# Kernel optimization log

Hardware: AMD Instinct MI355X
Metric: run time of the kernel (lower is better)

Reference implementation:

```python
import jax, jax.numpy as jnp
import numpy as np
from jax import lax

HUMAN_SIZE = 54
NUM_ACTIONS = 1
INPUT_SIZE = HUMAN_SIZE + NUM_ACTIONS  # 55, one_hot=True
RNN_SIZE = 1024
SOURCE_SEQ_LEN = 50
TARGET_SEQ_LEN = 25
BATCH = 1024


def setup_inputs() -> dict:
    key = jax.random.key(0)
    ks = jax.random.split(key, 8)
    s = 1.0 / np.sqrt(RNN_SIZE)
    return {
        "encoder_inputs": jax.random.normal(ks[0], (BATCH, SOURCE_SEQ_LEN, INPUT_SIZE), jnp.float32),
        "decoder_inputs": jax.random.normal(ks[1], (BATCH, TARGET_SEQ_LEN, INPUT_SIZE), jnp.float32),
        "W_ih": jax.random.uniform(ks[2], (3 * RNN_SIZE, INPUT_SIZE), jnp.float32, -s, s),
        "W_hh": jax.random.uniform(ks[3], (3 * RNN_SIZE, RNN_SIZE), jnp.float32, -s, s),
        "b_ih": jax.random.uniform(ks[4], (3 * RNN_SIZE,), jnp.float32, -s, s),
        "b_hh": jax.random.uniform(ks[5], (3 * RNN_SIZE,), jnp.float32, -s, s),
        "fc_w": jax.random.uniform(ks[6], (INPUT_SIZE, RNN_SIZE), jnp.float32, -s, s),
        "fc_b": jax.random.uniform(ks[7], (INPUT_SIZE,), jnp.float32, -s, s),
    }


def _gru_step(h, x, W_ih, W_hh, b_ih, b_hh):
    # torch.nn.GRUCell math
    gi = x @ W_ih.T + b_ih            # [B, 3H]
    gh = h @ W_hh.T + b_hh            # [B, 3H]
    i_r, i_z, i_n = jnp.split(gi, 3, axis=-1)
    h_r, h_z, h_n = jnp.split(gh, 3, axis=-1)
    r = jax.nn.sigmoid(i_r + h_r)
    z = jax.nn.sigmoid(i_z + h_z)
    n = jnp.tanh(i_n + r * h_n)
    return (1.0 - z) * n + z * h


def reference(encoder_inputs, decoder_inputs, W_ih, W_hh, b_ih, b_hh, fc_w, fc_b):
    B = encoder_inputs.shape[0]
    H = W_hh.shape[1]
    state0 = jnp.zeros((B, H), dtype=encoder_inputs.dtype)

    # Encoder: first source_seq_len-1 frames, time-major scan (dropout p=0 -> identity)
    enc_tm = jnp.swapaxes(encoder_inputs[:, : SOURCE_SEQ_LEN - 1], 0, 1)  # [S-1, B, In]

    def enc_step(h, x):
        return _gru_step(h, x, W_ih, W_hh, b_ih, b_hh), None

    state, _ = lax.scan(enc_step, state0, enc_tm)

    def dec_step(carry, _):
        h, inp = carry
        inp = lax.stop_gradient(inp)  # inp.detach()
        h = _gru_step(h, inp, W_ih, W_hh, b_ih, b_hh)
        out = inp + h @ fc_w.T + fc_b  # residual add
        return (h, out), out

    (_, _), outs = lax.scan(dec_step, (state, decoder_inputs[:, 0]), None, length=TARGET_SEQ_LEN)
    return jnp.swapaxes(outs, 0, 1)  # [B, T, In]
```

## Files before the change

### kernel.cpp

```cpp
#include <hip/hip_runtime.h>


typedef unsigned short ushort_t;
typedef __bf16 bf16x8 __attribute__((ext_vector_type(8)));
typedef float f32x4 __attribute__((ext_vector_type(4)));
typedef unsigned int u32x4 __attribute__((ext_vector_type(4)));

#define MFMA(a, b, c) __builtin_amdgcn_mfma_f32_16x16x32_bf16(a, b, c, 0, 0, 0)

static __device__ __forceinline__ ushort_t f2bf(float f) {
  union { float f; unsigned u; } x; x.f = f;
  unsigned r = x.u + 0x7fffu + ((x.u >> 16) & 1u);
  return (ushort_t)(r >> 16);
}
static __device__ __forceinline__ float sigmf(float x) { return 1.f / (1.f + __expf(-x)); }
static __device__ __forceinline__ float tanhf_(float x) { return 1.f - 2.f / (__expf(2.f * x) + 1.f); }

static __device__ __forceinline__ __amdgpu_buffer_rsrc_t mkrsrc(const void* p) {
  return __builtin_amdgcn_make_buffer_rsrc(const_cast<void*>(p), (short)0, -1, 0x00020000);
}
#if __has_builtin(__builtin_amdgcn_raw_buffer_load_b128)
static __device__ __forceinline__ bf16x8 ldb(__amdgpu_buffer_rsrc_t r, int voff) {
  u32x4 v = __builtin_amdgcn_raw_buffer_load_b128(r, voff, 0, 1);
  union { u32x4 u; bf16x8 b; } x; x.u = v; return x.b;
}
static __device__ __forceinline__ bf16x8 ldbc(__amdgpu_buffer_rsrc_t r, int voff) {
  u32x4 v = __builtin_amdgcn_raw_buffer_load_b128(r, voff, 0, 0);
  union { u32x4 u; bf16x8 b; } x; x.u = v; return x.b;
}
#else
static __device__ __forceinline__ bf16x8 ldb(__amdgpu_buffer_rsrc_t r, int voff) {
  union { unsigned u[4]; bf16x8 b; } x;
  x.u[0] = __builtin_amdgcn_raw_buffer_load_b32(r, voff, 0, 1);
  x.u[1] = __builtin_amdgcn_raw_buffer_load_b32(r, voff + 4, 0, 1);
  x.u[2] = __builtin_amdgcn_raw_buffer_load_b32(r, voff + 8, 0, 1);
  x.u[3] = __builtin_amdgcn_raw_buffer_load_b32(r, voff + 12, 0, 1);
  return x.b;
}
static __device__ __forceinline__ bf16x8 ldbc(__amdgpu_buffer_rsrc_t r, int voff) {
  union { unsigned u[4]; bf16x8 b; } x;
  x.u[0] = __builtin_amdgcn_raw_buffer_load_b32(r, voff, 0, 0);
  x.u[1] = __builtin_amdgcn_raw_buffer_load_b32(r, voff + 4, 0, 0);
  x.u[2] = __builtin_amdgcn_raw_buffer_load_b32(r, voff + 8, 0, 0);
  x.u[3] = __builtin_amdgcn_raw_buffer_load_b32(r, voff + 12, 0, 0);
  return x.b;
}
#endif

__global__ __launch_bounds__(512, 2)
void seq2seq_xcd(const float* __restrict__ enc, const float* __restrict__ dec,
                 const float* __restrict__ Wih, const float* __restrict__ Whh,
                 const float* __restrict__ b_ih, const float* __restrict__ b_hh,
                 const float* __restrict__ fcw, const float* __restrict__ fcb,
                 float* __restrict__ outp,
                 ushort_t* __restrict__ xg, ushort_t* __restrict__ hA,
                 ushort_t* __restrict__ innA, ushort_t* __restrict__ nG,
                 ushort_t* __restrict__ fcG, unsigned* cnt) {
  __shared__ ushort_t WrzL[65536];
  __shared__ ushort_t WiL[6144];
  __shared__ float scratchF[4096];
  __shared__ unsigned sgs;

  const int tid = threadIdx.x;
  const int w = tid >> 6, l = tid & 63;
  const int fr = l & 15, fq4 = l >> 4;

  if (tid == 0) {
    unsigned x;
    asm volatile("s_getreg_b32 %0, hwreg(HW_REG_XCC_ID, 0, 8)" : "=s"(x));
    x &= 7u;
    unsigned s = atomicAdd(&cnt[x * 64], 1u);
    sgs = (x << 8) | s;
  }
  __syncthreads();
  const int g = sgs >> 8, slot = sgs & 255;
  const bool isFC = (slot >= 24);

  unsigned* arr4 = cnt + (8 + g * 4 + (slot & 3)) * 64;
  unsigned* arrb = cnt + (8 + g * 4) * 64;
  auto fcpp = [&](int td) { return cnt + (48 + g * 25 + td) * 64; };

  ushort_t* hbase = hA + (size_t)g * 262144;
  auto hb = [&](int i) { return hbase + (size_t)i * 131072; };
  ushort_t* xgg = xg + (size_t)g * 49 * 8192;
  auto inng = [&](int i) { return innA + (size_t)(g * 2 + i) * 8192; };
  ushort_t* nGp = nG + (size_t)(g * 32 + slot) * 32768;
  ushort_t* fcGg = fcG + (size_t)g * 65536;

  for (int i = tid; i < 65536; i += 512) {
    int j = i & 7, ln = (i >> 3) & 63, jf = (i >> 9) & 1, gt = (i >> 10) & 1, kt = i >> 11;
    int col = gt * 1024 + slot * 32 + jf * 16 + (ln & 15);
    int k = kt * 32 + (ln >> 4) * 8 + j;
    WrzL[i] = f2bf(Whh[(size_t)col * 1024 + k]);
  }
  for (int i = tid; i < 6144; i += 512) {
    int j = i & 7, ln = (i >> 3) & 63, jf = (i >> 9) & 1, rem = i >> 10;
    int gt = rem % 3, kt = rem / 3;
    int col = gt * 1024 + slot * 32 + jf * 16 + (ln & 15);
    int k = kt * 32 + (ln >> 4) * 8 + j;
    WiL[i] = (k < 55) ? f2bf(Wih[(size_t)col * 55 + k]) : (ushort_t)0;
  }
  for (int i = tid; i < 32768; i += 512) {
    int j = i & 7, ln = (i >> 3) & 63, jf = (i >> 9) & 1, kt = i >> 10;
    int col = 2048 + slot * 32 + jf * 16 + (ln & 15);
    int k = kt * 32 + (ln >> 4) * 8 + j;
    nGp[i] = f2bf(Whh[(size_t)col * 1024 + k]);
  }
#pragma unroll
  for (int rep = 0; rep < 2; ++rep) {
    int t = slot + rep * 32;
    if (t < 49) {
      ushort_t* xp = xgg + (size_t)t * 8192;
      for (int i = tid; i < 8192; i += 512) {
        int sub = i & 7, row = (i >> 3) & 127, kc = i >> 10;
        int c = kc * 8 + sub;
        xp[i] = (c < 55) ? f2bf(enc[((size_t)(g * 128 + row) * 50 + t) * 55 + c]) : (ushort_t)0;
      }
    }
  }
  if (slot < 4) {
    ushort_t* ip = inng(0);
    for (int i = slot * 2048 + tid; i < (slot + 1) * 2048; i += 512) {
      int sub = i & 7, row = (i >> 3) & 127, kc = i >> 10;
      int c = kc * 8 + sub;
      ip[i] = (c < 55) ? f2bf(dec[(size_t)(g * 128 + row) * 1375 + c]) : (ushort_t)0;
    }
  }
  if (isFC) {
    for (int i = (slot - 24) * 8192 + tid; i < (slot - 23) * 8192; i += 512) {
      int j = i & 7, ln = (i >> 3) & 63, jf = (i >> 9) & 3, kt = i >> 11;
      int c = jf * 16 + (ln & 15);
      int k = kt * 32 + (ln >> 4) * 8 + j;
      fcGg[i] = (c < 55) ? f2bf(fcw[(size_t)c * 1024 + k]) : (ushort_t)0;
    }
  }

  float brz[2], bzz[2], bin[2], bhn[2];
#pragma unroll
  for (int jf = 0; jf < 2; ++jf) {
    int col = slot * 32 + jf * 16 + fr;
    brz[jf] = b_ih[col] + b_hh[col];
    bzz[jf] = b_ih[1024 + col] + b_hh[1024 + col];
    bin[jf] = b_ih[2048 + col];
    bhn[jf] = b_hh[2048 + col];
  }
  const int Rfc = (slot - 24) * 16;
  const int jfF = w & 3;
  const int colF = jfF * 16 + fr;
  float fcbF = 0.f, inp[4] = {0.f, 0.f, 0.f, 0.f};
  if (isFC && w < 4) {
    fcbF = (colF < 55) ? fcb[colF] : 0.f;
#pragma unroll
    for (int v = 0; v < 4; ++v)
      inp[v] = (colF < 55) ? dec[(size_t)(g * 128 + Rfc + fq4 * 4 + v) * 1375 + colF] : 0.f;
  }
  f32x4 hreg0 = (f32x4){0.f, 0.f, 0.f, 0.f};
  f32x4 hreg1 = (f32x4){0.f, 0.f, 0.f, 0.f};

  auto arrive = [&]() {
    __syncthreads();
    if (tid == 0) atomicAdd(arr4, 1u);
  };
  auto wait_rel = [&](unsigned k) {
    if (tid == 0) {
      for (;;) {
        unsigned s0 = __hip_atomic_load(arrb, __ATOMIC_RELAXED, __HIP_MEMORY_SCOPE_AGENT);
        unsigned s1 = __hip_atomic_load(arrb + 64, __ATOMIC_RELAXED, __HIP_MEMORY_SCOPE_AGENT);
        unsigned s2 = __hip_atomic_load(arrb + 128, __ATOMIC_RELAXED, __HIP_MEMORY_SCOPE_AGENT);
        unsigned s3 = __hip_atomic_load(arrb + 192, __ATOMIC_RELAXED, __HIP_MEMORY_SCOPE_AGENT);
        if (s0 + s1 + s2 + s3 >= 32u * k) break;
        __builtin_amdgcn_s_sleep(1);
      }
    }
    __syncthreads();
  };
  auto fc_wait = [&](int td) {
    if (tid == 0) {
      while (__hip_atomic_load(fcpp(td), __ATOMIC_RELAXED, __HIP_MEMORY_SCOPE_AGENT) < 8u)
        __builtin_amdgcn_s_sleep(1);
    }
    __syncthreads();
  };

  f32x4 av[12], nx0, nx1;
  bf16x8 pA0[4], pA1[4];
  bf16x8 pN0[4], pN1[4];
  bf16x8 pb0, pb1, pb2, pb3;

  __amdgpu_buffer_rsrc_t rnG = mkrsrc(nGp);

  auto xpart = [&](const ushort_t* xp) {
    __amdgpu_buffer_rsrc_t rx = mkrsrc(xp);
    const int R = (w & 3) * 32 + (w >> 2) * 16;
#pragma unroll
    for (int kt = 0; kt < 2; ++kt) {
      bf16x8 a = ldb(rx, ((kt * 4 + fq4) * 128 + R + fr) * 16);
      const ushort_t* bl = WiL + kt * 3072 + l * 8;
      bf16x8 br_0 = *(const bf16x8*)(bl);
      bf16x8 br_1 = *(const bf16x8*)(bl + 512);
      bf16x8 bz_0 = *(const bf16x8*)(bl + 1024);
      bf16x8 bz_1 = *(const bf16x8*)(bl + 1536);
      bf16x8 bn_0 = *(const bf16x8*)(bl + 2048);
      bf16x8 bn_1 = *(const bf16x8*)(bl + 2560);
      if (w < 4) {
        av[0] = MFMA(a, br_0, av[0]);
        av[1] = MFMA(a, br_1, av[1]);
        av[4] = MFMA(a, bz_0, av[4]);
        av[5] = MFMA(a, bz_1, av[5]);
      } else {
        av[2] = MFMA(a, br_0, av[2]);
        av[3] = MFMA(a, br_1, av[3]);
        av[6] = MFMA(a, bz_0, av[6]);
        av[7] = MFMA(a, bz_1, av[7]);
      }
      nx0 = MFMA(a, bn_0, nx0);
      nx1 = MFMA(a, bn_1, nx1);
    }
  };

  auto hpre = [&]() {
    const int kh = w >> 2;
#pragma unroll
    for (int i = 0; i < 4; ++i) {
      int kt = kh * 16 + i;
      pN0[i] = ldbc(rnG, kt * 2048 + l * 16);
      pN1[i] = ldbc(rnG, kt * 2048 + 1024 + l * 16);
    }
    const ushort_t* bl0 = WrzL + (kh * 16) * 2048 + l * 8;
    pb0 = *(const bf16x8*)(bl0);
    pb1 = *(const bf16x8*)(bl0 + 512);
    pb2 = *(const bf16x8*)(bl0 + 1024);
    pb3 = *(const bf16x8*)(bl0 + 1536);
  };

  auto hmain = [&](const ushort_t* hbp) {
    __amdgpu_buffer_rsrc_t r = mkrsrc(hbp);
    const int kh = w >> 2, R = (w & 3) * 32;
#pragma unroll
    for (int i = 0; i < 4; ++i) {
      int kt = kh * 16 + i;
      pA0[i] = ldb(r, ((kt * 4 + fq4) * 128 + R + fr) * 16);
      pA1[i] = ldb(r, ((kt * 4 + fq4) * 128 + R + 16 + fr) * 16);
    }
    bf16x8 br0 = pb0, br1 = pb1, bz0 = pb2, bz1 = pb3;
#pragma unroll
    for (int i = 0; i < 16; ++i) {
      int kt = kh * 16 + i;
      bf16x8 a0 = pA0[i & 3], a1 = pA1[i & 3];
      bf16x8 n0 = pN0[i & 3], n1 = pN1[i & 3];
      bf16x8 cr0 = br0, cr1 = br1, cz0 = bz0, cz1 = bz1;
      if (i < 15) {
        const ushort_t* bln = WrzL + (kt + 1) * 2048 + l * 8;
        br0 = *(const bf16x8*)(bln);
        br1 = *(const bf16x8*)(bln + 512);
        bz0 = *(const bf16x8*)(bln + 1024);
        bz1 = *(const bf16x8*)(bln + 1536);
      }
      if (i < 12) {
        int kp = kt + 4;
        pA0[i & 3] = ldb(r, ((kp * 4 + fq4) * 128 + R + fr) * 16);
        pA1[i & 3] = ldb(r, ((kp * 4 + fq4) * 128 + R + 16 + fr) * 16);
        pN0[i & 3] = ldbc(rnG, kp * 2048 + l * 16);
        pN1[i & 3] = ldbc(rnG, kp * 2048 + 1024 + l * 16);
      }
      av[0] = MFMA(a0, cr0, av[0]);
      av[2] = MFMA(a1, cr0, av[2]);
      av[1] = MFMA(a0, cr1, av[1]);
      av[3] = MFMA(a1, cr1, av[3]);
      av[4] = MFMA(a0, cz0, av[4]);
      av[6] = MFMA(a1, cz0, av[6]);
      av[5] = MFMA(a0, cz1, av[5]);
      av[7] = MFMA(a1, cz1, av[7]);
      av[8] = MFMA(a0, n0, av[8]);
      av[10] = MFMA(a1, n0, av[10]);
      av[9] = MFMA(a0, n1, av[9]);
      av[11] = MFMA(a1, n1, av[11]);
    }
  };

#define KXCH(LO0, LO1, HI0, HI1, TS)                                \
  do {                                                              \
    if (w >= 4) {                                                   \
      float* sp_ = scratchF + ((w - 4) * 64 + l) * 4;               \
      *(f32x4*)(sp_) = av[LO0];                                     \
      *(f32x4*)(sp_ + 1024) = av[LO1];                              \
    } else {                                                        \
      float* sp_ = scratchF + (w * 64 + l) * 4;                     \
      *(f32x4*)(sp_ + 2048) = av[HI0];                              \
      *(f32x4*)(sp_ + 3072) = av[HI1];                              \
    }                                                               \
    __syncthreads();                                                \
    if (w < 4) {                                                    \
      const float* sp_ = scratchF + (w * 64 + l) * 4;               \
      av[LO0] += *(const f32x4*)(sp_);                              \
      av[LO1] += *(const f32x4*)(sp_ + 1024);                       \
    } else {                                                        \
      const float* sp_ = scratchF + ((w - 4) * 64 + l) * 4;         \
      av[HI0] += *(const f32x4*)(sp_ + 2048);                       \
      av[HI1] += *(const f32x4*)(sp_ + 3072);                       \
    }                                                               \
    if (TS) __syncthreads();                                        \
  } while (0)

#define EPI(RV, ZV, NHV, NXV, JF, HC)                                  \
  do {                                                                 \
    const int kq_ = slot * 4 + (JF)*2 + (fr >> 3);                     \
    _Pragma("unroll") for (int v = 0; v < 4; ++v) {                    \
      float rr = sigmf(RV[v] + brz[JF]);                               \
      float zz = sigmf(ZV[v] + bzz[JF]);                               \
      float nn = tanhf_(NXV[v] + bin[JF] + rr * (NHV[v] + bhn[JF]));   \
      float h = (1.f - zz) * nn + zz * HC[v];                          \
      HC[v] = h;                                                       \
      int row_ = Rbase + fq4 * 4 + v;                                  \
      hn[(kq_ * 128 + row_) * 8 + sub_] = f2bf(h);                     \
    }                                                                  \
  } while (0)

  auto fcdo = [&](const ushort_t* hbp, int td, bool wr, ushort_t* innW) {
    __amdgpu_buffer_rsrc_t r = mkrsrc(hbp);
    __amdgpu_buffer_rsrc_t rf = mkrsrc(fcGg);
    const int kh = w >> 2;
    f32x4 fa = (f32x4){0.f, 0.f, 0.f, 0.f};
    bf16x8 Af[4], Bf[4];
#pragma unroll
    for (int i = 0; i < 4; ++i) {
      int kt = kh * 16 + i;
      Af[i] = ldb(r, ((kt * 4 + fq4) * 128 + Rfc + fr) * 16);
      Bf[i] = ldbc(rf, (kt * 4 + jfF) * 1024 + l * 16);
    }
#pragma unroll
    for (int i = 0; i < 16; ++i) {
      int kt = kh * 16 + i;
      bf16x8 a = Af[i & 3], bb = Bf[i & 3];
      if (i < 12) {
        Af[i & 3] = ldb(r, (((kt + 4) * 4 + fq4) * 128 + Rfc + fr) * 16);
        Bf[i & 3] = ldbc(rf, ((kt + 4) * 4 + jfF) * 1024 + l * 16);
      }
      fa = MFMA(a, bb, fa);
    }
    if (w >= 4) *(f32x4*)(scratchF + ((w - 4) * 64 + l) * 4) = fa;
    __syncthreads();
    if (w < 4) {
      fa += *(const f32x4*)(scratchF + (w * 64 + l) * 4);
      const int kq = colF >> 3, sub = colF & 7;
#pragma unroll
      for (int v = 0; v < 4; ++v) {
        int row = Rfc + fq4 * 4 + v;
        float o = fa[v] + inp[v] + fcbF;
        inp[v] = o;
        if (wr) innW[(kq * 128 + row) * 8 + sub] = f2bf(o);
        if (colF < 55) outp[(size_t)(g * 128 + row) * 1375 + td * 55 + colF] = o;
      }
    }
    __syncthreads();
  };

  arrive();
  wait_rel(1);

  for (int t = 0; t < 74; ++t) {
#pragma unroll
    for (int i = 0; i < 12; ++i) av[i] = (f32x4){0.f, 0.f, 0.f, 0.f};
    nx0 = (f32x4){0.f, 0.f, 0.f, 0.f};
    nx1 = (f32x4){0.f, 0.f, 0.f, 0.f};

    if (t <= 49) {
      xpart(t <= 48 ? xgg + (size_t)t * 8192 : inng(0));
    }
    if (t > 0) {
      hpre();
      wait_rel(t + 1);
    }
    if (t >= 50 && isFC) {
      fcdo(hb(t & 1), t - 50, true, inng((t - 49) & 1));
      if (tid == 0) atomicAdd(fcpp(t - 50), 1u);
    }
    if (t > 0) hmain(hb(t & 1));
    if (t >= 50) {
      fc_wait(t - 50);
      xpart(inng((t - 49) & 1));
    }
    KXCH(0, 1, 2, 3, 1);
    KXCH(4, 5, 6, 7, 1);
    KXCH(8, 9, 10, 11, 0);
    {
      ushort_t* hn = hb((t + 1) & 1);
      const int Rbase = (w & 3) * 32 + (w >> 2) * 16;
      const int sub_ = fr & 7;
      if (w < 4) {
        EPI(av[0], av[4], av[8], nx0, 0, hreg0);
        EPI(av[1], av[5], av[9], nx1, 1, hreg1);
      } else {
        EPI(av[2], av[6], av[10], nx0, 0, hreg0);
        EPI(av[3], av[7], av[11], nx1, 1, hreg1);
      }
    }
    arrive();
  }

  if (isFC) {
    wait_rel(75);
    fcdo(hb(0), 24, false, (ushort_t*)0);
  }
}

extern "C" void kernel_launch(void* const* d_in, const int* in_sizes, int n_in,
                              void* d_out, int out_size, void* d_ws, size_t ws_size,
                              hipStream_t stream) {
  const float* enc  = (const float*)d_in[0];
  const float* dec  = (const float*)d_in[1];
  const float* Wih  = (const float*)d_in[2];
  const float* Whh  = (const float*)d_in[3];
  const float* b_ih = (const float*)d_in[4];
  const float* b_hh = (const float*)d_in[5];
  const float* fcw  = (const float*)d_in[6];
  const float* fcb  = (const float*)d_in[7];
  float* out = (float*)d_out;

  char* ws = (char*)d_ws;
  unsigned* cnt  = (unsigned*)ws; ws += 65536;
  ushort_t* xg   = (ushort_t*)ws; ws += (size_t)8 * 49 * 8192 * 2;
  ushort_t* hA   = (ushort_t*)ws; ws += (size_t)8 * 2 * 131072 * 2;
  ushort_t* innA = (ushort_t*)ws; ws += (size_t)8 * 2 * 8192 * 2;
  ushort_t* nG   = (ushort_t*)ws; ws += (size_t)8 * 32 * 32768 * 2;
  ushort_t* fcG  = (ushort_t*)ws; ws += (size_t)8 * 65536 * 2;

  (void)hipMemsetAsync(cnt, 0, 65536, stream);
  seq2seq_xcd<<<256, 512, 0, stream>>>(
      enc, dec, Wih, Whh, b_ih, b_hh, fcw, fcb, out,
      xg, hA, innA, nG, fcG, cnt);
}
```

Before: 781.6 us.

## Spread decoder FC projection across all 32 blocks per group instead of 8

The decoder's output projection (h @ fc_w) was computed only by the 8 FC-designated blocks per batch group, each doing a 16-row tile with K split across two wave halves. Now every block in the group computes a 16x16 output tile with K split across all 8 waves and reduced through scratch, and the FC-done counter waits for 32 arrivals. This shortens the per-step critical path of the serial FC, which the next step's input depends on. In exchange every block does extra FC work, an 8-way LDS reduction, and more atomics per step.

```diff
diff --git a/kernel.cpp b/kernel.cpp
--- a/kernel.cpp
+++ b/kernel.cpp
@@ -144,15 +144,15 @@
     bin[jf] = b_ih[2048 + col];
     bhn[jf] = b_hh[2048 + col];
   }
-  const int Rfc = (slot - 24) * 16;
-  const int jfF = w & 3;
-  const int colF = jfF * 16 + fr;
-  float fcbF = 0.f, inp[4] = {0.f, 0.f, 0.f, 0.f};
-  if (isFC && w < 4) {
-    fcbF = (colF < 55) ? fcb[colF] : 0.f;
+  const int Rm = (slot >> 2) * 16;
+  const int cn = slot & 3;
+  const int colO = cn * 16 + fr;
+  float fcbO = 0.f, inpO[4] = {0.f, 0.f, 0.f, 0.f};
+  if (w == 0) {
+    fcbO = (colO < 55) ? fcb[colO] : 0.f;
 #pragma unroll
     for (int v = 0; v < 4; ++v)
-      inp[v] = (colF < 55) ? dec[(size_t)(g * 128 + Rfc + fq4 * 4 + v) * 1375 + colF] : 0.f;
+      inpO[v] = (colO < 55) ? dec[(size_t)(g * 128 + Rm + fq4 * 4 + v) * 1375 + colO] : 0.f;
   }
   f32x4 hreg0 = (f32x4){0.f, 0.f, 0.f, 0.f};
   f32x4 hreg1 = (f32x4){0.f, 0.f, 0.f, 0.f};
@@ -176,7 +176,7 @@
   };
   auto fc_wait = [&](int td) {
     if (tid == 0) {
-      while (__hip_atomic_load(fcpp(td), __ATOMIC_RELAXED, __HIP_MEMORY_SCOPE_AGENT) < 8u)
+      while (__hip_atomic_load(fcpp(td), __ATOMIC_RELAXED, __HIP_MEMORY_SCOPE_AGENT) < 32u)
         __builtin_amdgcn_s_sleep(1);
     }
     __syncthreads();
@@ -316,40 +316,34 @@
     }                                                                  \
   } while (0)
 
-  auto fcdo = [&](const ushort_t* hbp, int td, bool wr, ushort_t* innW) {
+  auto fcdo32 = [&](const ushort_t* hbp, int td, bool wr, ushort_t* innW) {
     __amdgpu_buffer_rsrc_t r = mkrsrc(hbp);
     __amdgpu_buffer_rsrc_t rf = mkrsrc(fcGg);
-    const int kh = w >> 2;
+    bf16x8 Af[4], Bf[4];
+#pragma unroll
+    for (int i = 0; i < 4; ++i) {
+      int kt = w * 4 + i;
+      Af[i] = ldb(r, ((kt * 4 + fq4) * 128 + Rm + fr) * 16);
+      Bf[i] = ldbc(rf, (kt * 4 + cn) * 1024 + l * 16);
+    }
     f32x4 fa = (f32x4){0.f, 0.f, 0.f, 0.f};
-    bf16x8 Af[4], Bf[4];
-#pragma unroll
-    for (int i = 0; i < 4; ++i) {
-      int kt = kh * 16 + i;
-      Af[i] = ldb(r, ((kt * 4 + fq4) * 128 + Rfc + fr) * 16);
-      Bf[i] = ldbc(rf, (kt * 4 + jfF) * 1024 + l * 16);
-    }
-#pragma unroll
-    for (int i = 0; i < 16; ++i) {
-      int kt = kh * 16 + i;
-      bf16x8 a = Af[i & 3], bb = Bf[i & 3];
-      if (i < 12) {
-        Af[i & 3] = ldb(r, (((kt + 4) * 4 + fq4) * 128 + Rfc + fr) * 16);
-        Bf[i & 3] = ldbc(rf, ((kt + 4) * 4 + jfF) * 1024 + l * 16);
-      }
-      fa = MFMA(a, bb, fa);
-    }
-    if (w >= 4) *(f32x4*)(scratchF + ((w - 4) * 64 + l) * 4) = fa;
+#pragma unroll
+    for (int i = 0; i < 4; ++i) fa = MFMA(Af[i], Bf[i], fa);
+    *(f32x4*)(scratchF + (w * 64 + l) * 4) = fa;
     __syncthreads();
-    if (w < 4) {
-      fa += *(const f32x4*)(scratchF + (w * 64 + l) * 4);
-      const int kq = colF >> 3, sub = colF & 7;
+    if (w == 0) {
+      f32x4 s = *(const f32x4*)(scratchF + l * 4);
+#pragma unroll
+      for (int ww = 1; ww < 8; ++ww)
+        s += *(const f32x4*)(scratchF + (ww * 64 + l) * 4);
+      const int kq = colO >> 3, sub = colO & 7;
 #pragma unroll
       for (int v = 0; v < 4; ++v) {
-        int row = Rfc + fq4 * 4 + v;
-        float o = fa[v] + inp[v] + fcbF;
-        inp[v] = o;
+        int row = Rm + fq4 * 4 + v;
+        float o = s[v] + inpO[v] + fcbO;
+        inpO[v] = o;
         if (wr) innW[(kq * 128 + row) * 8 + sub] = f2bf(o);
-        if (colF < 55) outp[(size_t)(g * 128 + row) * 1375 + td * 55 + colF] = o;
+        if (colO < 55) outp[(size_t)(g * 128 + row) * 1375 + td * 55 + colO] = o;
       }
     }
     __syncthreads();
@@ -371,8 +365,8 @@
       hpre();
       wait_rel(t + 1);
     }
-    if (t >= 50 && isFC) {
-      fcdo(hb(t & 1), t - 50, true, inng((t - 49) & 1));
+    if (t >= 50) {
+      fcdo32(hb(t & 1), t - 50, true, inng((t - 49) & 1));
       if (tid == 0) atomicAdd(fcpp(t - 50), 1u);
     }
     if (t > 0) hmain(hb(t & 1));
@@ -398,10 +392,8 @@
     arrive();
   }
 
-  if (isFC) {
-    wait_rel(75);
-    fcdo(hb(0), 24, false, (ushort_t*)0);
-  }
+  wait_rel(75);
+  fcdo32(hb(0), 24, false, (ushort_t*)0);
 }
 
 extern "C" void kernel_launch(void* const* d_in, const int* in_sizes, int n_in,
```

Result: faster. 754.2 us, median of 2 (-3.5%).
